# Performance work log

Measured on AMD Instinct MI355X. Metric: run time of the kernel, lower is better.

Reference implementation:

```python
import jax, jax.numpy as jnp
import numpy as np

NUM_CLASSES = 21
THRESHOLD = 0.5
VAR0, VAR1 = 0.1, 0.2
NEGPOS_RATIO = 3


def setup_inputs() -> dict:
    key = jax.random.key(0)
    k1, k2, k3, k4, k5, k6, k7 = jax.random.split(key, 7)
    B, P, C, O = 64, 8732, 21, 8
    loc_data = jax.random.normal(k1, (B, P, 4), dtype=jnp.float32) * 0.1
    conf_data = jax.random.normal(k2, (B, P, C), dtype=jnp.float32)
    # priors: center form (cx, cy, w, h), valid in [0,1]
    cxy = jax.random.uniform(k3, (P, 2), minval=0.05, maxval=0.95)
    pwh = jax.random.uniform(k4, (P, 2), minval=0.05, maxval=0.3)
    priors = jnp.concatenate([cxy, pwh], axis=-1).astype(jnp.float32)
    # targets: corner-form boxes + class label (float), (B, O, 5)
    tc = jax.random.uniform(k5, (B, O, 2), minval=0.2, maxval=0.8)
    twh = jax.random.uniform(k6, (B, O, 2), minval=0.1, maxval=0.4)
    tmin = jnp.clip(tc - twh / 2, 0.0, 1.0)
    tmax = jnp.clip(tc + twh / 2, 0.0, 1.0)
    labels = jax.random.randint(k7, (B, O, 1), 0, C - 1).astype(jnp.float32)
    targets = jnp.concatenate([tmin, tmax, labels], axis=-1)
    return {"loc_data": loc_data, "conf_data": conf_data, "priors": priors, "targets": targets}


def _point_form(p):
    # (cx,cy,w,h) -> (xmin,ymin,xmax,ymax)
    return jnp.concatenate([p[:, :2] - p[:, 2:] / 2, p[:, :2] + p[:, 2:] / 2], axis=-1)


def _jaccard(a, b):
    # a: (O,4) corners, b: (P,4) corners -> (O,P)
    lt = jnp.maximum(a[:, None, :2], b[None, :, :2])
    rb = jnp.minimum(a[:, None, 2:], b[None, :, 2:])
    wh = jnp.clip(rb - lt, 0.0, None)
    inter = wh[..., 0] * wh[..., 1]
    area_a = ((a[:, 2] - a[:, 0]) * (a[:, 3] - a[:, 1]))[:, None]
    area_b = ((b[:, 2] - b[:, 0]) * (b[:, 3] - b[:, 1]))[None, :]
    return inter / (area_a + area_b - inter)


def _match_one(truths, labels, priors_pt, priors):
    # truths: (O,4) corners, labels: (O,), priors: (P,4) center-form
    ov = _jaccard(truths, priors_pt)                      # (O,P)
    best_prior_idx = jnp.argmax(ov, axis=1)               # (O,)
    best_truth_overlap = jnp.max(ov, axis=0)              # (P,)
    best_truth_idx = jnp.argmax(ov, axis=0)               # (P,)
    # ensure every gt box matches its best prior
    best_truth_overlap = best_truth_overlap.at[best_prior_idx].set(2.0)
    best_truth_idx = best_truth_idx.at[best_prior_idx].set(jnp.arange(truths.shape[0]))
    matched = truths[best_truth_idx]                      # (P,4)
    conf = labels[best_truth_idx].astype(jnp.int32) + 1
    conf = jnp.where(best_truth_overlap < THRESHOLD, 0, conf)
    # encode offsets
    g_cxcy = ((matched[:, :2] + matched[:, 2:]) / 2 - priors[:, :2]) / (VAR0 * priors[:, 2:])
    g_wh = jnp.log(jnp.clip((matched[:, 2:] - matched[:, :2]) / priors[:, 2:], 1e-8, None)) / VAR1
    return jnp.concatenate([g_cxcy, g_wh], axis=-1), conf


def _forward(loc_data, conf_data, priors, targets):
    B, P, C = conf_data.shape
    priors_sg = jax.lax.stop_gradient(priors)             # torch uses .data
    targets_sg = jax.lax.stop_gradient(targets)
    priors_pt = _point_form(priors_sg)
    loc_t, conf_t = jax.vmap(_match_one, in_axes=(0, 0, None, None))(
        targets_sg[:, :, :4], targets_sg[:, :, 4], priors_pt, priors_sg)
    pos = conf_t > 0                                      # (B,P)

    # localization: smooth L1 summed over positive priors
    diff = loc_data - loc_t
    ad = jnp.abs(diff)
    sl1 = jnp.where(ad < 1.0, 0.5 * diff * diff, ad - 0.5)
    loss_l = jnp.sum(sl1 * pos[..., None].astype(sl1.dtype))

    # per-prior conf loss for hard negative mining
    lse = jax.nn.logsumexp(conf_data, axis=-1)            # (B,P)
    gathered = jnp.take_along_axis(conf_data, conf_t[..., None], axis=-1)[..., 0]
    loss_c_all = lse - gathered                           # (B,P)
    mined = jnp.where(pos, 0.0, loss_c_all)
    loss_idx = jnp.argsort(-mined, axis=1)                # descending
    idx_rank = jnp.argsort(loss_idx, axis=1)
    num_pos = jnp.sum(pos.astype(jnp.int32), axis=1, keepdims=True)  # (B,1)
    num_neg = jnp.minimum(NEGPOS_RATIO * num_pos, P - num_pos)
    neg = idx_rank < num_neg                              # (B,P)

    sel = (pos | neg).astype(loss_c_all.dtype)
    loss_c = jnp.sum(loss_c_all * sel)

    N = jnp.sum(num_pos).astype(loss_l.dtype)
    return loss_l / N, loss_c / N


def reference(loc_data, conf_data, priors, targets):
    return _forward(loc_data, conf_data, priors, targets)
```

## Files before the change

### kernel.cpp

```cpp
#include <hip/hip_runtime.h>
#include <math.h>

#define TPB 256
#define CHP 512
#define TPBS 1024
#define RCAP 12

__device__ __forceinline__ float jac(float tx0, float ty0, float tx1, float ty1, float ta,
                                     float px0, float py0, float px1, float py1, float pa) {
    float ltx = fmaxf(tx0, px0), lty = fmaxf(ty0, py0);
    float rbx = fminf(tx1, px1), rby = fminf(ty1, py1);
    float w = fmaxf(rbx - ltx, 0.0f), h = fmaxf(rby - lty, 0.0f);
    float inter = w * h;
    return inter / (ta + pa - inter);
}

template <int ON>
__global__ __launch_bounds__(TPB) void match1_kernel(
    const float* __restrict__ priors, const float* __restrict__ targets,
    int P, int O_rt, int S1, unsigned long long* __restrict__ pkeys) {
    constexpr int OMAX = (ON > 0) ? ON : 64;
    const int O = (ON > 0) ? ON : O_rt;
    const int b = blockIdx.x / S1;
    const int chunk = blockIdx.x % S1;
    const int p0 = chunk * CHP;
    const int p1 = min(p0 + CHP, P);
    const int tid = threadIdx.x;
    const int lane = tid & 63, wv = tid >> 6;

    __shared__ float s_tx0[OMAX], s_ty0[OMAX], s_tx1[OMAX], s_ty1[OMAX], s_area[OMAX];
    __shared__ unsigned long long s_wk[TPB / 64][OMAX];
    for (int o = tid; o < O; o += TPB) {
        const float* t = targets + ((size_t)b * O + o) * 5;
        float x0 = t[0], y0 = t[1], x1 = t[2], y1 = t[3];
        s_tx0[o] = x0; s_ty0[o] = y0; s_tx1[o] = x1; s_ty1[o] = y1;
        s_area[o] = (x1 - x0) * (y1 - y0);
    }
    __syncthreads();

    unsigned long long k[OMAX];
    for (int o = 0; o < O; ++o) k[o] = 0ull;
    for (int p = p0 + tid; p < p1; p += TPB) {
        float4 pr = ((const float4*)priors)[p];
        float px0 = pr.x - pr.z * 0.5f, py0 = pr.y - pr.w * 0.5f;
        float px1 = pr.x + pr.z * 0.5f, py1 = pr.y + pr.w * 0.5f;
        float pa = (px1 - px0) * (py1 - py0);
        for (int o = 0; o < O; ++o) {
            float ov = jac(s_tx0[o], s_ty0[o], s_tx1[o], s_ty1[o], s_area[o],
                           px0, py0, px1, py1, pa);
            unsigned long long kk =
                ((unsigned long long)__float_as_uint(ov) << 32) |
                (unsigned long long)(0xFFFFFFFFu - (unsigned)p);
            if (kk > k[o]) k[o] = kk;
        }
    }
    for (int o = 0; o < O; ++o) {
        unsigned long long kk = k[o];
        for (int off = 32; off > 0; off >>= 1) {
            unsigned long long other = __shfl_down(kk, off, 64);
            if (other > kk) kk = other;
        }
        if (lane == 0) s_wk[wv][o] = kk;
    }
    __syncthreads();
    if (tid < O) {
        unsigned long long kk = s_wk[0][tid];
        for (int w = 1; w < TPB / 64; ++w)
            if (s_wk[w][tid] > kk) kk = s_wk[w][tid];
        pkeys[((size_t)b * O + tid) * S1 + chunk] = kk;
    }
}

template <int ON, int CN>
__global__ __launch_bounds__(TPB) void match2_conf_kernel(
    const float* __restrict__ loc, const float* __restrict__ priors,
    const float* __restrict__ targets, const float* __restrict__ conf,
    const unsigned long long* __restrict__ pkeys,
    int P, int O_rt, int C_rt, int S1, int CB,
    float* __restrict__ mined, float* __restrict__ part_ll,
    float* __restrict__ part_pc, int* __restrict__ part_np) {
    constexpr int OMAX = (ON > 0) ? ON : 64;
    const int O = (ON > 0) ? ON : O_rt;
    const int C = (CN > 0) ? CN : C_rt;
    const int b = blockIdx.x / CB;
    const int chunk = blockIdx.x % CB;
    const int r0 = chunk * TPB;
    const int n = min(TPB, P - r0);
    const int tid = threadIdx.x;

    __shared__ float s_rows[TPB * ((CN > 0) ? CN : 32)];
    __shared__ float s_tx0[OMAX], s_ty0[OMAX], s_tx1[OMAX], s_ty1[OMAX];
    __shared__ float s_lab[OMAX], s_area[OMAX];
    __shared__ unsigned long long s_keys[OMAX];
    __shared__ int s_bp[OMAX];
    __shared__ float s_f[TPB], s_g[TPB];
    __shared__ int s_i[TPB];

    for (int o = tid; o < O; o += TPB) {
        const float* t = targets + ((size_t)b * O + o) * 5;
        float x0 = t[0], y0 = t[1], x1 = t[2], y1 = t[3];
        s_tx0[o] = x0; s_ty0[o] = y0; s_tx1[o] = x1; s_ty1[o] = y1;
        s_lab[o] = t[4];
        s_area[o] = (x1 - x0) * (y1 - y0);
        s_keys[o] = 0ull;
    }
    __syncthreads();

    if (tid < O * S1) {
        int o = tid / S1, s = tid % S1;
        atomicMax(&s_keys[o], pkeys[((size_t)b * O + o) * S1 + s]);
    }
    {
        const float* g = conf + ((size_t)b * P + r0) * C;
        const int nf = n * C;
        if ((((size_t)g) & 15) == 0) {
            const int nf4 = nf >> 2;
            const float4* g4 = (const float4*)g;
            float4* s4 = (float4*)s_rows;
            for (int i = tid; i < nf4; i += TPB) s4[i] = g4[i];
            for (int i = (nf4 << 2) + tid; i < nf; i += TPB) s_rows[i] = g[i];
        } else {
            for (int i = tid; i < nf; i += TPB) s_rows[i] = g[i];
        }
    }
    __syncthreads();
    if (tid < O)
        s_bp[tid] = (int)(0xFFFFFFFFu - (unsigned)(s_keys[tid] & 0xFFFFFFFFull));
    __syncthreads();

    float ll = 0.0f, posc = 0.0f;
    int np = 0;
    if (tid < n) {
        const int p = r0 + tid;
        float4 pr = ((const float4*)priors)[p];
        float cx = pr.x, cy = pr.y, pw = pr.z, ph = pr.w;
        float px0 = cx - pw * 0.5f, py0 = cy - ph * 0.5f;
        float px1 = cx + pw * 0.5f, py1 = cy + ph * 0.5f;
        float pa = (px1 - px0) * (py1 - py0);
        float bto = -1.0f;
        int bti = 0;
        for (int o = 0; o < O; ++o) {
            float ov = jac(s_tx0[o], s_ty0[o], s_tx1[o], s_ty1[o], s_area[o],
                           px0, py0, px1, py1, pa);
            if (ov > bto) { bto = ov; bti = o; }
        }
        for (int o = 0; o < O; ++o) {
            if (s_bp[o] == p) { bto = 2.0f; bti = o; }
        }
        int c = (bto < 0.5f) ? 0 : ((int)s_lab[bti] + 1);

        const float* row = s_rows + tid * C;
        float m = row[0];
        for (int j = 1; j < C; ++j) m = fmaxf(m, row[j]);
        float s = 0.0f;
        for (int j = 0; j < C; ++j) s += expf(row[j] - m);
        float lse = m + logf(s);
        float lc = lse - row[c];
        bool pos = c > 0;
        mined[(size_t)b * P + p] = pos ? 0.0f : lc;
        if (pos) {
            posc = lc;
            np = 1;
            float mx0 = s_tx0[bti], my0 = s_ty0[bti], mx1 = s_tx1[bti], my1 = s_ty1[bti];
            float g0 = ((mx0 + mx1) * 0.5f - cx) / (0.1f * pw);
            float g1 = ((my0 + my1) * 0.5f - cy) / (0.1f * ph);
            float g2 = logf(fmaxf((mx1 - mx0) / pw, 1e-8f)) / 0.2f;
            float g3 = logf(fmaxf((my1 - my0) / ph, 1e-8f)) / 0.2f;
            float4 ld = ((const float4*)loc)[(size_t)b * P + p];
            float gt4[4] = {g0, g1, g2, g3};
            float lv[4] = {ld.x, ld.y, ld.z, ld.w};
#pragma unroll
            for (int j = 0; j < 4; ++j) {
                float d = lv[j] - gt4[j];
                float ad = fabsf(d);
                ll += (ad < 1.0f) ? 0.5f * d * d : (ad - 0.5f);
            }
        }
    }
    __syncthreads();
    s_f[tid] = ll; s_g[tid] = posc; s_i[tid] = np;
    __syncthreads();
    for (int s = TPB / 2; s > 0; s >>= 1) {
        if (tid < s) {
            s_f[tid] += s_f[tid + s];
            s_g[tid] += s_g[tid + s];
            s_i[tid] += s_i[tid + s];
        }
        __syncthreads();
    }
    if (tid == 0) {
        part_ll[blockIdx.x] = s_f[0];
        part_pc[blockIdx.x] = s_g[0];
        part_np[blockIdx.x] = s_i[0];
    }
}

__global__ __launch_bounds__(TPBS) void select_kernel(
    const float* __restrict__ mined, const float* __restrict__ part_ll,
    const float* __restrict__ part_pc, const int* __restrict__ part_np,
    float* __restrict__ ll_batch, float* __restrict__ lc_batch,
    int* __restrict__ np_batch, int P, int CB, int ratio) {
    const int b = blockIdx.x, tid = threadIdx.x;
    const int wv = tid >> 6;
    constexpr int W = TPBS / 64;
    const float* v = mined + (size_t)b * P;
    const int NIT = (P + TPBS - 1) / TPBS;
    const bool cached = (NIT <= RCAP);

    __shared__ float s_rs[TPBS];
    __shared__ int s_rc[TPBS];
    __shared__ int s_hist[W * 256];
    __shared__ int s_scan[257];
    __shared__ unsigned s_bsel;
    __shared__ int s_krn;

    float rv[RCAP];
    if (cached) {
        for (int it = 0; it < NIT; ++it) {
            int p = tid + it * TPBS;
            rv[it] = (p < P) ? v[p] : 0.0f;
        }
    }

    float pll = 0.0f, ppc = 0.0f;
    int pnp = 0;
    for (int i = tid; i < CB; i += TPBS) {
        pll += part_ll[b * CB + i];
        ppc += part_pc[b * CB + i];
        pnp += part_np[b * CB + i];
    }
    s_rs[tid] = pll; s_rc[tid] = pnp;
    __syncthreads();
    for (int s = TPBS / 2; s > 0; s >>= 1) {
        if (tid < s) { s_rs[tid] += s_rs[tid + s]; s_rc[tid] += s_rc[tid + s]; }
        __syncthreads();
    }
    const float ll_sum = s_rs[0];
    const int npos = s_rc[0];
    __syncthreads();
    s_rs[tid] = ppc;
    __syncthreads();
    for (int s = TPBS / 2; s > 0; s >>= 1) {
        if (tid < s) s_rs[tid] += s_rs[tid + s];
        __syncthreads();
    }
    const float sum_pos = s_rs[0];
    __syncthreads();

    const int k = min(ratio * npos, P - npos);
    if (tid == 0) {
        ll_batch[b] = ll_sum;
        np_batch[b] = npos;
    }
    if (k <= 0) {
        if (tid == 0) lc_batch[b] = sum_pos;
        return;
    }

    unsigned prefix = 0u;
    int kr = k;
    for (int pass = 0; pass < 4; ++pass) {
        const int shift = 24 - 8 * pass;
        const unsigned mask = (pass == 0) ? 0u : (0xFFFFFFFFu << (32 - 8 * pass));
        for (int i = tid; i < W * 256; i += TPBS) s_hist[i] = 0;
        __syncthreads();
        for (int it = 0; it < NIT; ++it) {
            int p = tid + it * TPBS;
            if (p < P) {
                unsigned u = __float_as_uint(cached ? rv[it] : v[p]);
                if ((u & mask) == prefix)
                    atomicAdd(&s_hist[wv * 256 + ((u >> shift) & 0xFF)], 1);
            }
        }
        __syncthreads();
        if (tid < 256) {
            int h = 0;
            for (int w = 0; w < W; ++w) h += s_hist[w * 256 + tid];
            s_scan[tid] = h;
        }
        if (tid == 0) s_scan[256] = 0;
        __syncthreads();
        for (int d = 1; d < 256; d <<= 1) {
            int val = 0;
            if (tid < 256) val = s_scan[tid] + ((tid + d < 256) ? s_scan[tid + d] : 0);
            __syncthreads();
            if (tid < 256) s_scan[tid] = val;
            __syncthreads();
        }
        if (tid < 256) {
            int sge = s_scan[tid];
            int sgt = s_scan[tid + 1];
            if (sge >= kr && sgt < kr) {
                s_bsel = (unsigned)tid;
                s_krn = kr - sgt;
            }
        }
        __syncthreads();
        prefix |= s_bsel << shift;
        kr = s_krn;
        __syncthreads();
    }
    const float T = __uint_as_float(prefix);
    float lsum = 0.0f;
    int lcnt = 0;
    for (int it = 0; it < NIT; ++it) {
        int p = tid + it * TPBS;
        if (p < P) {
            float x = cached ? rv[it] : v[p];
            if (x > T) { lsum += x; ++lcnt; }
        }
    }
    s_rs[tid] = lsum; s_rc[tid] = lcnt;
    __syncthreads();
    for (int s = TPBS / 2; s > 0; s >>= 1) {
        if (tid < s) { s_rs[tid] += s_rs[tid + s]; s_rc[tid] += s_rc[tid + s]; }
        __syncthreads();
    }
    if (tid == 0) lc_batch[b] = sum_pos + s_rs[0] + (float)(k - s_rc[0]) * T;
}

__global__ __launch_bounds__(TPB) void finalize_kernel(
    const float* __restrict__ ll_batch, const int* __restrict__ np_batch,
    const float* __restrict__ lc_batch, int B, float* __restrict__ out) {
    const int tid = threadIdx.x;
    __shared__ float s_l[TPB], s_c[TPB];
    __shared__ int s_n[TPB];
    float l = 0.0f, c = 0.0f;
    int n = 0;
    for (int i = tid; i < B; i += TPB) {
        l += ll_batch[i];
        c += lc_batch[i];
        n += np_batch[i];
    }
    s_l[tid] = l; s_c[tid] = c; s_n[tid] = n;
    __syncthreads();
    for (int s = TPB / 2; s > 0; s >>= 1) {
        if (tid < s) {
            s_l[tid] += s_l[tid + s];
            s_c[tid] += s_c[tid + s];
            s_n[tid] += s_n[tid + s];
        }
        __syncthreads();
    }
    if (tid == 0) {
        float N = (float)s_n[0];
        out[0] = s_l[0] / N;
        out[1] = s_c[0] / N;
    }
}

extern "C" void kernel_launch(void* const* d_in, const int* in_sizes, int n_in,
                              void* d_out, int out_size, void* d_ws, size_t ws_size,
                              hipStream_t stream) {
    const float* loc = (const float*)d_in[0];
    const float* conf = (const float*)d_in[1];
    const float* priors = (const float*)d_in[2];
    const float* targets = (const float*)d_in[3];

    const int P = in_sizes[2] / 4;
    const int B = in_sizes[0] / (P * 4);
    const int C = in_sizes[1] / (in_sizes[0] / 4);
    const int O = in_sizes[3] / (B * 5);
    const size_t BP = (size_t)B * P;
    const int S1 = (P + CHP - 1) / CHP;
    const int CB = (P + TPB - 1) / TPB;

    unsigned long long* pkeys = (unsigned long long*)d_ws;
    float* mined = (float*)(pkeys + (size_t)B * O * S1);
    float* part_ll = mined + BP;
    float* part_pc = part_ll + (size_t)B * CB;
    int* part_np = (int*)(part_pc + (size_t)B * CB);
    float* ll_batch = (float*)(part_np + (size_t)B * CB);
    float* lc_batch = ll_batch + B;
    int* np_batch = (int*)(lc_batch + B);

    if (O == 8) {
        match1_kernel<8><<<B * S1, TPB, 0, stream>>>(priors, targets, P, O, S1, pkeys);
        if (C == 21) {
            match2_conf_kernel<8, 21><<<B * CB, TPB, 0, stream>>>(
                loc, priors, targets, conf, pkeys, P, O, C, S1, CB,
                mined, part_ll, part_pc, part_np);
        } else {
            match2_conf_kernel<8, 0><<<B * CB, TPB, 0, stream>>>(
                loc, priors, targets, conf, pkeys, P, O, C, S1, CB,
                mined, part_ll, part_pc, part_np);
        }
    } else {
        match1_kernel<0><<<B * S1, TPB, 0, stream>>>(priors, targets, P, O, S1, pkeys);
        match2_conf_kernel<0, 0><<<B * CB, TPB, 0, stream>>>(
            loc, priors, targets, conf, pkeys, P, O, C, S1, CB,
            mined, part_ll, part_pc, part_np);
    }

    select_kernel<<<B, TPBS, 0, stream>>>(mined, part_ll, part_pc, part_np,
                                          ll_batch, lc_batch, np_batch, P, CB, 3);

    finalize_kernel<<<1, TPB, 0, stream>>>(ll_batch, np_batch, lc_batch, B,
                                           (float*)d_out);
}
```

Measured before the change: 137.6 us.

## Process each prior with a 16-lane group using shuffle reductions instead of shared staging

The match2/conf kernel now gives each prior to a 16-lane subgroup. Each lane reads up to two class logits straight from global memory, and logsumexp, the best-truth argmax and the label-logit gather are done with subgroup shuffles. This removes the large shared-memory staging of conf rows and the serial per-thread loop over classes. The block reduction now uses wavefront shuffles instead of a shared-memory tree. In exchange, global loads become strided per lane (each 84-byte row is read by 16 lanes), only one lane per group does the positive work, and C is capped at 32 by the two-register layout.

```diff
diff --git a/kernel.cpp b/kernel.cpp
--- a/kernel.cpp
+++ b/kernel.cpp
@@ -5,6 +5,9 @@
 #define CHP 512
 #define TPBS 1024
 #define RCAP 12
+#define ROWIT 8
+
+typedef unsigned long long ull;
 
 __device__ __forceinline__ float jac(float tx0, float ty0, float tx1, float ty1, float ta,
                                      float px0, float py0, float px1, float py1, float pa) {
@@ -18,7 +21,7 @@
 template <int ON>
 __global__ __launch_bounds__(TPB) void match1_kernel(
     const float* __restrict__ priors, const float* __restrict__ targets,
-    int P, int O_rt, int S1, unsigned long long* __restrict__ pkeys) {
+    int P, int O_rt, int S1, ull* __restrict__ pkeys) {
     constexpr int OMAX = (ON > 0) ? ON : 64;
     const int O = (ON > 0) ? ON : O_rt;
     const int b = blockIdx.x / S1;
@@ -29,7 +32,7 @@
     const int lane = tid & 63, wv = tid >> 6;
 
     __shared__ float s_tx0[OMAX], s_ty0[OMAX], s_tx1[OMAX], s_ty1[OMAX], s_area[OMAX];
-    __shared__ unsigned long long s_wk[TPB / 64][OMAX];
+    __shared__ ull s_wk[TPB / 64][OMAX];
     for (int o = tid; o < O; o += TPB) {
         const float* t = targets + ((size_t)b * O + o) * 5;
         float x0 = t[0], y0 = t[1], x1 = t[2], y1 = t[3];
@@ -38,7 +41,7 @@
     }
     __syncthreads();
 
-    unsigned long long k[OMAX];
+    ull k[OMAX];
     for (int o = 0; o < O; ++o) k[o] = 0ull;
     for (int p = p0 + tid; p < p1; p += TPB) {
         float4 pr = ((const float4*)priors)[p];
@@ -48,53 +51,51 @@
         for (int o = 0; o < O; ++o) {
             float ov = jac(s_tx0[o], s_ty0[o], s_tx1[o], s_ty1[o], s_area[o],
                            px0, py0, px1, py1, pa);
-            unsigned long long kk =
-                ((unsigned long long)__float_as_uint(ov) << 32) |
-                (unsigned long long)(0xFFFFFFFFu - (unsigned)p);
+            ull kk = ((ull)__float_as_uint(ov) << 32) |
+                     (ull)(0xFFFFFFFFu - (unsigned)p);
             if (kk > k[o]) k[o] = kk;
         }
     }
     for (int o = 0; o < O; ++o) {
-        unsigned long long kk = k[o];
+        ull kk = k[o];
         for (int off = 32; off > 0; off >>= 1) {
-            unsigned long long other = __shfl_down(kk, off, 64);
+            ull other = __shfl_down(kk, off, 64);
             if (other > kk) kk = other;
         }
         if (lane == 0) s_wk[wv][o] = kk;
     }
     __syncthreads();
     if (tid < O) {
-        unsigned long long kk = s_wk[0][tid];
+        ull kk = s_wk[0][tid];
         for (int w = 1; w < TPB / 64; ++w)
             if (s_wk[w][tid] > kk) kk = s_wk[w][tid];
         pkeys[((size_t)b * O + tid) * S1 + chunk] = kk;
     }
 }
 
-template <int ON, int CN>
-__global__ __launch_bounds__(TPB) void match2_conf_kernel(
+template <int ON>
+__global__ __launch_bounds__(TPB) void m2c_kernel(
     const float* __restrict__ loc, const float* __restrict__ priors,
     const float* __restrict__ targets, const float* __restrict__ conf,
-    const unsigned long long* __restrict__ pkeys,
-    int P, int O_rt, int C_rt, int S1, int CB,
+    const ull* __restrict__ pkeys,
+    int P, int O_rt, int C, int S1, int CB2,
     float* __restrict__ mined, float* __restrict__ part_ll,
     float* __restrict__ part_pc, int* __restrict__ part_np) {
     constexpr int OMAX = (ON > 0) ? ON : 64;
     const int O = (ON > 0) ? ON : O_rt;
-    const int C = (CN > 0) ? CN : C_rt;
-    const int b = blockIdx.x / CB;
-    const int chunk = blockIdx.x % CB;
-    const int r0 = chunk * TPB;
-    const int n = min(TPB, P - r0);
+    const int b = blockIdx.x / CB2;
+    const int chunk = blockIdx.x % CB2;
+    const int r0 = chunk * (16 * ROWIT);
     const int tid = threadIdx.x;
-
-    __shared__ float s_rows[TPB * ((CN > 0) ? CN : 32)];
+    const int j = tid & 15;
+    const int gidx = tid >> 4;
+
     __shared__ float s_tx0[OMAX], s_ty0[OMAX], s_tx1[OMAX], s_ty1[OMAX];
     __shared__ float s_lab[OMAX], s_area[OMAX];
-    __shared__ unsigned long long s_keys[OMAX];
+    __shared__ ull s_keys[OMAX];
     __shared__ int s_bp[OMAX];
-    __shared__ float s_f[TPB], s_g[TPB];
-    __shared__ int s_i[TPB];
+    __shared__ float s_wll[TPB / 64], s_wpc[TPB / 64];
+    __shared__ int s_wnp[TPB / 64];
 
     for (int o = tid; o < O; o += TPB) {
         const float* t = targets + ((size_t)b * O + o) * 5;
@@ -105,93 +106,114 @@
         s_keys[o] = 0ull;
     }
     __syncthreads();
-
     if (tid < O * S1) {
         int o = tid / S1, s = tid % S1;
         atomicMax(&s_keys[o], pkeys[((size_t)b * O + o) * S1 + s]);
     }
-    {
-        const float* g = conf + ((size_t)b * P + r0) * C;
-        const int nf = n * C;
-        if ((((size_t)g) & 15) == 0) {
-            const int nf4 = nf >> 2;
-            const float4* g4 = (const float4*)g;
-            float4* s4 = (float4*)s_rows;
-            for (int i = tid; i < nf4; i += TPB) s4[i] = g4[i];
-            for (int i = (nf4 << 2) + tid; i < nf; i += TPB) s_rows[i] = g[i];
-        } else {
-            for (int i = tid; i < nf; i += TPB) s_rows[i] = g[i];
-        }
-    }
     __syncthreads();
     if (tid < O)
         s_bp[tid] = (int)(0xFFFFFFFFu - (unsigned)(s_keys[tid] & 0xFFFFFFFFull));
     __syncthreads();
 
-    float ll = 0.0f, posc = 0.0f;
+    float ll = 0.0f, pc = 0.0f;
     int np = 0;
-    if (tid < n) {
-        const int p = r0 + tid;
-        float4 pr = ((const float4*)priors)[p];
-        float cx = pr.x, cy = pr.y, pw = pr.z, ph = pr.w;
-        float px0 = cx - pw * 0.5f, py0 = cy - ph * 0.5f;
-        float px1 = cx + pw * 0.5f, py1 = cy + ph * 0.5f;
-        float pa = (px1 - px0) * (py1 - py0);
-        float bto = -1.0f;
-        int bti = 0;
-        for (int o = 0; o < O; ++o) {
-            float ov = jac(s_tx0[o], s_ty0[o], s_tx1[o], s_ty1[o], s_area[o],
-                           px0, py0, px1, py1, pa);
-            if (ov > bto) { bto = ov; bti = o; }
-        }
-        for (int o = 0; o < O; ++o) {
-            if (s_bp[o] == p) { bto = 2.0f; bti = o; }
-        }
+
+    for (int it = 0; it < ROWIT; ++it) {
+        const int p = r0 + it * 16 + gidx;
+        const bool valid = (p < P);
+
+        float x0 = -INFINITY, x1 = -INFINITY;
+        if (valid) {
+            const float* row = conf + ((size_t)b * P + p) * C;
+            if (j < C) x0 = row[j];
+            if (j + 16 < C) x1 = row[j + 16];
+        }
+        float m = fmaxf(x0, x1);
+#pragma unroll
+        for (int d = 1; d < 16; d <<= 1) m = fmaxf(m, __shfl_xor(m, d, 16));
+        float e = expf(x0 - m) + expf(x1 - m);
+#pragma unroll
+        for (int d = 1; d < 16; d <<= 1) e += __shfl_xor(e, d, 16);
+        float lse = m + logf(e);
+
+        ull key = 0ull;
+        float cx = 0.f, cy = 0.f, pw = 1.f, ph = 1.f;
+        if (valid) {
+            float4 pr = ((const float4*)priors)[p];
+            cx = pr.x; cy = pr.y; pw = pr.z; ph = pr.w;
+            float px0 = cx - pw * 0.5f, py0 = cy - ph * 0.5f;
+            float px1 = cx + pw * 0.5f, py1 = cy + ph * 0.5f;
+            float pa = (px1 - px0) * (py1 - py0);
+            for (int o = j; o < O; o += 16) {
+                ull kk;
+                if (s_bp[o] == p) {
+                    kk = (0x40000000ull << 32) | (ull)(unsigned)o;
+                } else {
+                    float ov = jac(s_tx0[o], s_ty0[o], s_tx1[o], s_ty1[o], s_area[o],
+                                   px0, py0, px1, py1, pa);
+                    kk = ((ull)__float_as_uint(ov) << 32) | (ull)(unsigned)(255 - o);
+                }
+                if (kk > key) key = kk;
+            }
+        }
+#pragma unroll
+        for (int d = 1; d < 16; d <<= 1) {
+            ull kk2 = __shfl_xor(key, d, 16);
+            if (kk2 > key) key = kk2;
+        }
+        float bto = __uint_as_float((unsigned)(key >> 32));
+        int low = (int)(key & 0xFF);
+        int bti = (bto == 2.0f) ? low : (255 - low);
+        bti &= (OMAX > 16) ? 63 : 15;
         int c = (bto < 0.5f) ? 0 : ((int)s_lab[bti] + 1);
 
-        const float* row = s_rows + tid * C;
-        float m = row[0];
-        for (int j = 1; j < C; ++j) m = fmaxf(m, row[j]);
-        float s = 0.0f;
-        for (int j = 0; j < C; ++j) s += expf(row[j] - m);
-        float lse = m + logf(s);
-        float lc = lse - row[c];
-        bool pos = c > 0;
-        mined[(size_t)b * P + p] = pos ? 0.0f : lc;
-        if (pos) {
-            posc = lc;
-            np = 1;
-            float mx0 = s_tx0[bti], my0 = s_ty0[bti], mx1 = s_tx1[bti], my1 = s_ty1[bti];
-            float g0 = ((mx0 + mx1) * 0.5f - cx) / (0.1f * pw);
-            float g1 = ((my0 + my1) * 0.5f - cy) / (0.1f * ph);
-            float g2 = logf(fmaxf((mx1 - mx0) / pw, 1e-8f)) / 0.2f;
-            float g3 = logf(fmaxf((my1 - my0) / ph, 1e-8f)) / 0.2f;
-            float4 ld = ((const float4*)loc)[(size_t)b * P + p];
-            float gt4[4] = {g0, g1, g2, g3};
-            float lv[4] = {ld.x, ld.y, ld.z, ld.w};
+        int srcj = (c < 16) ? c : (c - 16);
+        float a0 = __shfl(x0, srcj, 16);
+        float a1 = __shfl(x1, srcj, 16);
+        float rowc = (c < 16) ? a0 : a1;
+        float lc = lse - rowc;
+
+        if (valid && j == 0) {
+            bool pos = c > 0;
+            mined[(size_t)b * P + p] = pos ? 0.0f : lc;
+            if (pos) {
+                pc += lc;
+                ++np;
+                float mx0 = s_tx0[bti], my0 = s_ty0[bti];
+                float mx1 = s_tx1[bti], my1 = s_ty1[bti];
+                float g0 = ((mx0 + mx1) * 0.5f - cx) / (0.1f * pw);
+                float g1 = ((my0 + my1) * 0.5f - cy) / (0.1f * ph);
+                float g2 = logf(fmaxf((mx1 - mx0) / pw, 1e-8f)) / 0.2f;
+                float g3 = logf(fmaxf((my1 - my0) / ph, 1e-8f)) / 0.2f;
+                float4 ld = ((const float4*)loc)[(size_t)b * P + p];
+                float gt4[4] = {g0, g1, g2, g3};
+                float lv[4] = {ld.x, ld.y, ld.z, ld.w};
 #pragma unroll
-            for (int j = 0; j < 4; ++j) {
-                float d = lv[j] - gt4[j];
-                float ad = fabsf(d);
-                ll += (ad < 1.0f) ? 0.5f * d * d : (ad - 0.5f);
+                for (int q = 0; q < 4; ++q) {
+                    float d = lv[q] - gt4[q];
+                    float ad = fabsf(d);
+                    ll += (ad < 1.0f) ? 0.5f * d * d : (ad - 0.5f);
+                }
             }
         }
     }
-    __syncthreads();
-    s_f[tid] = ll; s_g[tid] = posc; s_i[tid] = np;
-    __syncthreads();
-    for (int s = TPB / 2; s > 0; s >>= 1) {
-        if (tid < s) {
-            s_f[tid] += s_f[tid + s];
-            s_g[tid] += s_g[tid + s];
-            s_i[tid] += s_i[tid + s];
-        }
-        __syncthreads();
-    }
+
+#pragma unroll
+    for (int d = 1; d < 64; d <<= 1) {
+        ll += __shfl_xor(ll, d, 64);
+        pc += __shfl_xor(pc, d, 64);
+        np += __shfl_xor(np, d, 64);
+    }
+    const int wv = tid >> 6, lane = tid & 63;
+    if (lane == 0) { s_wll[wv] = ll; s_wpc[wv] = pc; s_wnp[wv] = np; }
+    __syncthreads();
     if (tid == 0) {
-        part_ll[blockIdx.x] = s_f[0];
-        part_pc[blockIdx.x] = s_g[0];
-        part_np[blockIdx.x] = s_i[0];
+        float L = 0.f, Pc = 0.f;
+        int N = 0;
+        for (int w = 0; w < TPB / 64; ++w) { L += s_wll[w]; Pc += s_wpc[w]; N += s_wnp[w]; }
+        part_ll[blockIdx.x] = L;
+        part_pc[blockIdx.x] = Pc;
+        part_np[blockIdx.x] = N;
     }
 }
 
@@ -363,37 +385,31 @@
     const int O = in_sizes[3] / (B * 5);
     const size_t BP = (size_t)B * P;
     const int S1 = (P + CHP - 1) / CHP;
-    const int CB = (P + TPB - 1) / TPB;
-
-    unsigned long long* pkeys = (unsigned long long*)d_ws;
+    const int CB2 = (P + 16 * ROWIT - 1) / (16 * ROWIT);
+
+    ull* pkeys = (ull*)d_ws;
     float* mined = (float*)(pkeys + (size_t)B * O * S1);
     float* part_ll = mined + BP;
-    float* part_pc = part_ll + (size_t)B * CB;
-    int* part_np = (int*)(part_pc + (size_t)B * CB);
-    float* ll_batch = (float*)(part_np + (size_t)B * CB);
+    float* part_pc = part_ll + (size_t)B * CB2;
+    int* part_np = (int*)(part_pc + (size_t)B * CB2);
+    float* ll_batch = (float*)(part_np + (size_t)B * CB2);
     float* lc_batch = ll_batch + B;
     int* np_batch = (int*)(lc_batch + B);
 
     if (O == 8) {
         match1_kernel<8><<<B * S1, TPB, 0, stream>>>(priors, targets, P, O, S1, pkeys);
-        if (C == 21) {
-            match2_conf_kernel<8, 21><<<B * CB, TPB, 0, stream>>>(
-                loc, priors, targets, conf, pkeys, P, O, C, S1, CB,
-                mined, part_ll, part_pc, part_np);
-        } else {
-            match2_conf_kernel<8, 0><<<B * CB, TPB, 0, stream>>>(
-                loc, priors, targets, conf, pkeys, P, O, C, S1, CB,
-                mined, part_ll, part_pc, part_np);
-        }
+        m2c_kernel<8><<<B * CB2, TPB, 0, stream>>>(
+            loc, priors, targets, conf, pkeys, P, O, C, S1, CB2,
+            mined, part_ll, part_pc, part_np);
     } else {
         match1_kernel<0><<<B * S1, TPB, 0, stream>>>(priors, targets, P, O, S1, pkeys);
-        match2_conf_kernel<0, 0><<<B * CB, TPB, 0, stream>>>(
-            loc, priors, targets, conf, pkeys, P, O, C, S1, CB,
+        m2c_kernel<0><<<B * CB2, TPB, 0, stream>>>(
+            loc, priors, targets, conf, pkeys, P, O, C, S1, CB2,
             mined, part_ll, part_pc, part_np);
     }
 
     select_kernel<<<B, TPBS, 0, stream>>>(mined, part_ll, part_pc, part_np,
-                                          ll_batch, lc_batch, np_batch, P, CB, 3);
+                                          ll_batch, lc_batch, np_batch, P, CB2, 3);
 
     finalize_kernel<<<1, TPB, 0, stream>>>(ll_batch, np_batch, lc_batch, B,
                                            (float*)d_out);
```

Measured after the change: 164.7 us. +19.7%, slower.
